# Kernel tuning notes

Hardware: AMD Instinct MI355X
Metric: run time of the kernel (lower is better)

Reference implementation:

```python
import jax, jax.numpy as jnp
import numpy as np

B, S, T = 16, 512, 16
P = 4  # unfold patch size / stride


def setup_inputs() -> dict:
    key = jax.random.key(0)
    k1, k2 = jax.random.split(key)
    inp = jax.random.normal(k1, (B, S, S, T), dtype=jnp.float32)
    n_patches = B * (S // P) * (S // P)
    # per-patch copy of the 16x6 projection, as in the expanded nn.Parameter
    fc_weight3 = jax.random.normal(k2, (n_patches, P * P, 6), dtype=jnp.float32) * 0.1
    return {"input": inp, "fc_weight3": fc_weight3}


def _interp_matrix(n_in, n_out):
    # 1D bilinear interpolation matrix with align_corners=True semantics
    coords = jnp.arange(n_out, dtype=jnp.float32) * ((n_in - 1) / (n_out - 1))
    i0 = jnp.clip(jnp.floor(coords).astype(jnp.int32), 0, n_in - 2)
    w = coords - i0.astype(jnp.float32)
    rows = jnp.arange(n_out)
    A = jnp.zeros((n_out, n_in), dtype=jnpp_dtype) if False else jnp.zeros((n_out, n_in), dtype=jnp.float32)
    A = A.at[rows, i0].add(1.0 - w).at[rows, i0 + 1].add(w)
    return A  # (n_out, n_in)


def reference(input, fc_weight3):
    b, s, _, t = input.shape
    g = s // P  # patch grid side
    # (b,s,s,t) -> (b,t,s,s), then extract non-overlapping 4x4 patches row-major
    x = jnp.transpose(input, (0, 3, 1, 2))
    x = x.reshape(b, t, g, P, g, P).transpose(0, 1, 2, 4, 3, 5)
    x = x.reshape(b, t, g, g, P * P)
    # (b,g,g,16,t) -> (N,16,t) -> (N,t,16)
    fm = x.transpose(0, 2, 3, 4, 1).reshape(-1, P * P, t).transpose(0, 2, 1)
    # per-patch CAM: bmm (N,t,16)@(N,16,6) then transpose -> (N,6,t)
    cam = jnp.einsum('ntk,nkm->nmt', fm, fc_weight3)
    cam = cam - jnp.min(cam, axis=2, keepdims=True)
    cam = cam / jnp.max(cam, axis=2, keepdims=True)
    # channel 0 only -> (b,t,g,g)
    top = cam[:, 0].reshape(b, g, g, t).transpose(0, 3, 1, 2)
    # bilinear upsample (g,g)->(s,s), align_corners=True, as two matmuls
    A = _interp_matrix(g, s)
    up = jnp.einsum('oi,btij,pj->btop', A, top, A)  # (b,t,s,s)
    return up.transpose(0, 2, 3, 1).reshape(-1, t)
```

## Files before the change

### kernel.cpp

```cpp
#include <hip/hip_runtime.h>

#define SDIM 512
#define GDIM 128
#define TDIM 16

__global__ __launch_bounds__(256) void cam_patch_kernel(const float* __restrict__ inp,
                                                        const float* __restrict__ w3,
                                                        float* __restrict__ top) {
    int n  = blockIdx.x * 16 + (threadIdx.x >> 4);
    int tt = threadIdx.x & 15;
    int b   = n >> 14;
    int rem = n & 16383;
    int gi  = rem >> 7;
    int gj  = rem & 127;

    float wlane = w3[n * 96 + tt * 6];

    float v = 0.f;
#pragma unroll
    for (int r = 0; r < 4; ++r) {
        const float* rowp = inp + ((size_t)((b * SDIM + gi * 4 + r) * SDIM + gj * 4) * TDIM) + tt;
#pragma unroll
        for (int c = 0; c < 4; ++c) {
            float wk = __shfl(wlane, r * 4 + c, 16);
            v += rowp[c * TDIM] * wk;
        }
    }

    float mn = v, mx = v;
#pragma unroll
    for (int off = 8; off >= 1; off >>= 1) {
        mn = fminf(mn, __shfl_xor(mn, off, 16));
        mx = fmaxf(mx, __shfl_xor(mx, off, 16));
    }
    float outv = (v - mn) / (mx - mn);

    top[((size_t)((b * GDIM + gi) * GDIM + gj) * TDIM) + tt] = outv;
}

__global__ __launch_bounds__(256) void upsample_kernel(const float* __restrict__ top,
                                                       float* __restrict__ out) {
    __shared__ float lds[2 * GDIM * TDIM];

    int b = blockIdx.x >> 9;
    int o = blockIdx.x & 511;

    const float scale = 127.0f / 511.0f;
    float ci = (float)o * scale;
    int i0 = (int)ci; if (i0 > GDIM - 2) i0 = GDIM - 2;
    float wi = ci - (float)i0;

    const float4* src = (const float4*)(top + (size_t)(b * GDIM + i0) * GDIM * TDIM);
    float4* dst = (float4*)lds;
#pragma unroll
    for (int idx = threadIdx.x; idx < 2 * GDIM * TDIM / 4; idx += 256)
        dst[idx] = src[idx];
    __syncthreads();

    size_t obase = (size_t)(b * SDIM + o) * SDIM * TDIM;
#pragma unroll
    for (int m = 0; m < 32; ++m) {
        int idx = m * 256 + threadIdx.x;
        int p  = idx >> 4;
        int tt = idx & 15;
        float cj = (float)p * scale;
        int j0 = (int)cj; if (j0 > GDIM - 2) j0 = GDIM - 2;
        float wj = cj - (float)j0;

        float a = lds[j0 * TDIM + tt];
        float bb = lds[j0 * TDIM + TDIM + tt];
        float c = lds[GDIM * TDIM + j0 * TDIM + tt];
        float d = lds[GDIM * TDIM + j0 * TDIM + TDIM + tt];
        float r0v = a + wj * (bb - a);
        float r1v = c + wj * (d - c);
        out[obase + idx] = r0v + wi * (r1v - r0v);
    }
}

extern "C" void kernel_launch(void* const* d_in, const int* in_sizes, int n_in,
                              void* d_out, int out_size, void* d_ws, size_t ws_size,
                              hipStream_t stream) {
    const float* inp = (const float*)d_in[0];
    const float* w3  = (const float*)d_in[1];
    float* out = (float*)d_out;
    float* top = (float*)d_ws;

    cam_patch_kernel<<<16384, 256, 0, stream>>>(inp, w3, top);
    upsample_kernel<<<8192, 256, 0, stream>>>(top, out);
}
```

Measured before the change: 512.7 us.

## Vectorize both kernels with float4 and pre-blend interpolation rows in LDS

```diff
diff --git a/kernel.cpp b/kernel.cpp
--- a/kernel.cpp
+++ b/kernel.cpp
@@ -7,73 +7,93 @@
 __global__ __launch_bounds__(256) void cam_patch_kernel(const float* __restrict__ inp,
                                                         const float* __restrict__ w3,
                                                         float* __restrict__ top) {
-    int n  = blockIdx.x * 16 + (threadIdx.x >> 4);
-    int tt = threadIdx.x & 15;
-    int b   = n >> 14;
-    int rem = n & 16383;
-    int gi  = rem >> 7;
-    int gj  = rem & 127;
+    const int t4 = threadIdx.x & 3;
+    const int pp = threadIdx.x >> 2;
+    const int n  = blockIdx.x * 64 + pp;
+    const int b  = n >> 14;
+    const int gi = (n >> 7) & 127;
+    const int gj = n & 127;
 
-    float wlane = w3[n * 96 + tt * 6];
+    const float* __restrict__ wp = w3 + (size_t)n * 96;
 
-    float v = 0.f;
+    float4 acc = make_float4(0.f, 0.f, 0.f, 0.f);
 #pragma unroll
     for (int r = 0; r < 4; ++r) {
-        const float* rowp = inp + ((size_t)((b * SDIM + gi * 4 + r) * SDIM + gj * 4) * TDIM) + tt;
+        const float* rowp = inp + ((size_t)((b * SDIM + gi * 4 + r) * SDIM + gj * 4) * TDIM) + t4 * 4;
 #pragma unroll
         for (int c = 0; c < 4; ++c) {
-            float wk = __shfl(wlane, r * 4 + c, 16);
-            v += rowp[c * TDIM] * wk;
+            const float wk = wp[(r * 4 + c) * 6];
+            const float4 x = *(const float4*)(rowp + c * TDIM);
+            acc.x += x.x * wk;
+            acc.y += x.y * wk;
+            acc.z += x.z * wk;
+            acc.w += x.w * wk;
         }
     }
 
-    float mn = v, mx = v;
-#pragma unroll
-    for (int off = 8; off >= 1; off >>= 1) {
-        mn = fminf(mn, __shfl_xor(mn, off, 16));
-        mx = fmaxf(mx, __shfl_xor(mx, off, 16));
-    }
-    float outv = (v - mn) / (mx - mn);
+    float mn = fminf(fminf(acc.x, acc.y), fminf(acc.z, acc.w));
+    float mx = fmaxf(fmaxf(acc.x, acc.y), fmaxf(acc.z, acc.w));
+    mn = fminf(mn, __shfl_xor(mn, 1, 4));
+    mx = fmaxf(mx, __shfl_xor(mx, 1, 4));
+    mn = fminf(mn, __shfl_xor(mn, 2, 4));
+    mx = fmaxf(mx, __shfl_xor(mx, 2, 4));
 
-    top[((size_t)((b * GDIM + gi) * GDIM + gj) * TDIM) + tt] = outv;
+    const float d = mx - mn;
+    float4 o;
+    o.x = (acc.x - mn) / d;
+    o.y = (acc.y - mn) / d;
+    o.z = (acc.z - mn) / d;
+    o.w = (acc.w - mn) / d;
+
+    *(float4*)(top + ((size_t)((b * GDIM + gi) * GDIM + gj) * TDIM) + t4 * 4) = o;
 }
 
 __global__ __launch_bounds__(256) void upsample_kernel(const float* __restrict__ top,
                                                        float* __restrict__ out) {
-    __shared__ float lds[2 * GDIM * TDIM];
+    __shared__ float4 lds[GDIM * TDIM / 4];
 
-    int b = blockIdx.x >> 9;
-    int o = blockIdx.x & 511;
+    const int b = blockIdx.x >> 9;
+    const int o = blockIdx.x & 511;
 
     const float scale = 127.0f / 511.0f;
-    float ci = (float)o * scale;
+    const float ci = (float)o * scale;
     int i0 = (int)ci; if (i0 > GDIM - 2) i0 = GDIM - 2;
-    float wi = ci - (float)i0;
+    const float wi = ci - (float)i0;
 
-    const float4* src = (const float4*)(top + (size_t)(b * GDIM + i0) * GDIM * TDIM);
-    float4* dst = (float4*)lds;
+    const float4* __restrict__ r0 = (const float4*)(top + (size_t)(b * GDIM + i0) * GDIM * TDIM);
+    const float4* __restrict__ r1 = r0 + GDIM * TDIM / 4;
 #pragma unroll
-    for (int idx = threadIdx.x; idx < 2 * GDIM * TDIM / 4; idx += 256)
-        dst[idx] = src[idx];
+    for (int it = 0; it < 2; ++it) {
+        const int idx = it * 256 + threadIdx.x;
+        const float4 a = r0[idx];
+        const float4 c = r1[idx];
+        float4 rb;
+        rb.x = a.x + wi * (c.x - a.x);
+        rb.y = a.y + wi * (c.y - a.y);
+        rb.z = a.z + wi * (c.z - a.z);
+        rb.w = a.w + wi * (c.w - a.w);
+        lds[idx] = rb;
+    }
     __syncthreads();
 
-    size_t obase = (size_t)(b * SDIM + o) * SDIM * TDIM;
+    float4* __restrict__ outp = (float4*)out + (size_t)(b * SDIM + o) * (SDIM * TDIM / 4);
 #pragma unroll
-    for (int m = 0; m < 32; ++m) {
-        int idx = m * 256 + threadIdx.x;
-        int p  = idx >> 4;
-        int tt = idx & 15;
-        float cj = (float)p * scale;
+    for (int it = 0; it < 8; ++it) {
+        const int idx4 = it * 256 + threadIdx.x;
+        const int p = idx4 >> 2;
+        const int q = idx4 & 3;
+        const float cj = (float)p * scale;
         int j0 = (int)cj; if (j0 > GDIM - 2) j0 = GDIM - 2;
-        float wj = cj - (float)j0;
+        const float wj = cj - (float)j0;
 
-        float a = lds[j0 * TDIM + tt];
-        float bb = lds[j0 * TDIM + TDIM + tt];
-        float c = lds[GDIM * TDIM + j0 * TDIM + tt];
-        float d = lds[GDIM * TDIM + j0 * TDIM + TDIM + tt];
-        float r0v = a + wj * (bb - a);
-        float r1v = c + wj * (d - c);
-        out[obase + idx] = r0v + wi * (r1v - r0v);
+        const float4 a  = lds[j0 * 4 + q];
+        const float4 bb = lds[j0 * 4 + 4 + q];
+        float4 v;
+        v.x = a.x + wj * (bb.x - a.x);
+        v.y = a.y + wj * (bb.y - a.y);
+        v.z = a.z + wj * (bb.z - a.z);
+        v.w = a.w + wj * (bb.w - a.w);
+        outp[idx4] = v;
     }
 }
 
@@ -85,6 +105,6 @@
     float* out = (float*)d_out;
     float* top = (float*)d_ws;
 
-    cam_patch_kernel<<<16384, 256, 0, stream>>>(inp, w3, top);
+    cam_patch_kernel<<<4096, 256, 0, stream>>>(inp, w3, top);
     upsample_kernel<<<8192, 256, 0, stream>>>(top, out);
 }
```

Result: slower. 523.5 us (+2.1%).
